# Performance work log

Measured on AMD Instinct MI355X. Metric: run time of the kernel, lower is better.

## Reference

```python
import jax, jax.numpy as jnp
from jax import lax
import numpy as np

DIM, HEADS, R = 256, 8, 2
B, H, W = 4, 64, 64
C = DIM // HEADS
SCALE = C ** -0.5


def setup_inputs() -> dict:
    key = jax.random.key(0)
    ks = jax.random.split(key, 6)
    s = 0.02
    x = jax.random.normal(ks[0], (B, DIM, H, W), dtype=jnp.float32)
    Wq = jax.random.normal(ks[1], (DIM, DIM), dtype=jnp.float32) * s
    Wkv = jax.random.normal(ks[2], (2 * DIM, DIM, R, R), dtype=jnp.float32) * s
    Wqb = jax.random.normal(ks[3], (DIM, DIM), dtype=jnp.float32) * s
    Wkvb = jax.random.normal(ks[4], (2 * DIM, DIM), dtype=jnp.float32) * s
    Wout = jax.random.normal(ks[5], (DIM, DIM), dtype=jnp.float32) * s
    return {"x": x, "Wq": Wq, "Wkv": Wkv, "Wqb": Wqb, "Wkvb": Wkvb, "Wout": Wout}


def _conv1x1(Wm, t):
    # 1x1 conv without bias == channel matmul
    return jnp.einsum('oc,bchw->bohw', Wm, t)


def reference(x, Wq, Wkv, Wqb, Wkvb, Wout):
    b, d, h, w = x.shape
    c = d // HEADS
    # ---- spatial-reduction branch ----
    q = _conv1x1(Wq, x)  # [b, d, h, w]
    kv = lax.conv_general_dilated(x, Wkv, (R, R), 'VALID',
                                  dimension_numbers=('NCHW', 'OIHW', 'NCHW'))
    k, v = jnp.split(kv, 2, axis=1)  # each [b, d, h/R, w/R]

    def to_img(t):
        bb, _, hh, ww = t.shape
        return t.reshape(bb, HEADS, c, hh * ww).transpose(0, 1, 3, 2).reshape(bb * HEADS, hh * ww, c)

    qi, ki, vi = to_img(q), to_img(k), to_img(v)
    attn_img = jax.nn.softmax(jnp.einsum('bid,bjd->bij', qi, ki) * SCALE, axis=-1)
    oi = jnp.einsum('bij,bjd->bid', attn_img, vi)  # [(b h), hw, c]
    out_img = oi.reshape(b, HEADS, h * w, c).transpose(0, 1, 3, 2).reshape(b, d, h, w)

    # ---- batch-wise branch ----
    qb = _conv1x1(Wqb, x)
    kvb = _conv1x1(Wkvb, x)
    kb, vb = jnp.split(kvb, 2, axis=1)

    def to_slice(t):
        # 'b (h c) x y -> (x y h) b c'
        return t.reshape(b, HEADS, c, h * w).transpose(3, 1, 0, 2).reshape(h * w * HEADS, b, c)

    qs, ks_, vs = to_slice(qb), to_slice(kb), to_slice(vb)
    attn_b = jax.nn.softmax(jnp.einsum('ibd,icd->ibc', qs, ks_) * SCALE, axis=-1)
    ob = jnp.einsum('ibc,icd->ibd', attn_b, vs)  # [(hw heads), b, c]
    out_batch = ob.reshape(h * w, HEADS, b, c).transpose(2, 1, 3, 0).reshape(b, d, h, w)

    return _conv1x1(Wout, out_img + out_batch)
```

## Files before the change

### kernel.cpp

```cpp
#include <hip/hip_runtime.h>

#define ATTN_SCALE 0.17677669529663687f

typedef __attribute__((ext_vector_type(8))) short bf16x8;
typedef __attribute__((ext_vector_type(4))) float f32x4;
typedef __attribute__((ext_vector_type(16))) float f32x16;

__device__ inline unsigned short f2bf(float x) {
    unsigned int u = __float_as_uint(x);
    unsigned int r = u + 0x7fffu + ((u >> 16) & 1u);
    return (unsigned short)(r >> 16);
}
__device__ inline unsigned int pk2(float lo, float hi) {
    return (unsigned int)f2bf(lo) | ((unsigned int)f2bf(hi) << 16);
}
__device__ inline float bf2f(unsigned int u) { return __uint_as_float(u << 16); }

#define GLDS16(gp, lp) \
    __builtin_amdgcn_global_load_lds((const __attribute__((address_space(1))) void*)(gp), \
                                     (__attribute__((address_space(3))) void*)(lp), 16, 0, 0)

__device__ inline void stage_tile(const ushort* __restrict__ g, int rstride, int kofs,
                                  ushort* lbase, int w, int lane) {
    const int r0 = w * 32;
    #pragma unroll
    for (int u = 0; u < 4; ++u) {
        const int row  = r0 + u * 8 + (lane >> 3);
        const int slog = (lane & 7) ^ (row & 7);
        GLDS16(g + (size_t)row * rstride + kofs + slog * 8,
               lbase + (size_t)(r0 + u * 8) * 64);
    }
}

__device__ inline bf16x8 frag_ld(const ushort* t, int row, int slog) {
    return *(const bf16x8*)(t + row * 64 + ((slog ^ (row & 7)) * 8));
}

#define MFMA_STEP(WS_, XS_, WM_, WP_)                                                       \
    _Pragma("unroll")                                                                       \
    for (int kh = 0; kh < 2; ++kh) {                                                        \
        bf16x8 av[4], bvv[4];                                                               \
        _Pragma("unroll")                                                                   \
        for (int fm = 0; fm < 4; ++fm) av[fm]  = frag_ld(WS_, WM_ + fm * 16 + i16, kh * 4 + g); \
        _Pragma("unroll")                                                                   \
        for (int fp = 0; fp < 4; ++fp) bvv[fp] = frag_ld(XS_, WP_ + fp * 16 + i16, kh * 4 + g); \
        _Pragma("unroll")                                                                   \
        for (int fm = 0; fm < 4; ++fm)                                                      \
            _Pragma("unroll")                                                               \
            for (int fp = 0; fp < 4; ++fp)                                                  \
                acc[fm][fp] = __builtin_amdgcn_mfma_f32_16x16x32_bf16(av[fm], bvv[fp],      \
                                                                      acc[fm][fp], 0, 0, 0); \
    }

__global__ __launch_bounds__(256) void cvt_x_kernel(
    const float* __restrict__ x, ushort* __restrict__ xbfT)
{
    __shared__ float T[64][65];
    const int t = threadIdx.x;
    const int p0 = blockIdx.x * 64, c0 = blockIdx.y * 64, bb = blockIdx.z;
    const float* xb = x + ((size_t)bb * 256 + c0) * 4096 + p0;
    {
        const int cc = t >> 2, pq = (t & 3) * 16;
        #pragma unroll
        for (int u = 0; u < 4; ++u) {
            const float4 v = *(const float4*)&xb[(size_t)cc * 4096 + pq + u * 4];
            T[cc][pq + u * 4 + 0] = v.x; T[cc][pq + u * 4 + 1] = v.y;
            T[cc][pq + u * 4 + 2] = v.z; T[cc][pq + u * 4 + 3] = v.w;
        }
    }
    __syncthreads();
    {
        const int pp = t >> 2, cq = (t & 3) * 16;
        uint4 w0, w1;
        w0.x = pk2(T[cq + 0][pp],  T[cq + 1][pp]);  w0.y = pk2(T[cq + 2][pp],  T[cq + 3][pp]);
        w0.z = pk2(T[cq + 4][pp],  T[cq + 5][pp]);  w0.w = pk2(T[cq + 6][pp],  T[cq + 7][pp]);
        w1.x = pk2(T[cq + 8][pp],  T[cq + 9][pp]);  w1.y = pk2(T[cq + 10][pp], T[cq + 11][pp]);
        w1.z = pk2(T[cq + 12][pp], T[cq + 13][pp]); w1.w = pk2(T[cq + 14][pp], T[cq + 15][pp]);
        ushort* dst = xbfT + ((size_t)bb * 4096 + p0 + pp) * 256 + c0 + cq;
        *(uint4*)&dst[0] = w0;
        *(uint4*)&dst[8] = w1;
    }
}

__global__ __launch_bounds__(256) void cvt_w_kernel(
    const float* __restrict__ Wq, const float* __restrict__ Wqb,
    const float* __restrict__ Wkvb, const float* __restrict__ Wkv,
    const float* __restrict__ Wout,
    ushort* __restrict__ Wallb, ushort* __restrict__ Wkvbb, ushort* __restrict__ Woutb)
{
    const int id = blockIdx.x * 256 + threadIdx.x;
    const float* src; ushort* dst;
    if (id < 65536) {
        const int m = id >> 6, c4 = (id & 63) * 4;
        src = (m < 256) ? &Wq[(size_t)m * 256 + c4]
            : (m < 512) ? &Wqb[(size_t)(m - 256) * 256 + c4]
                        : &Wkvb[(size_t)(m - 512) * 256 + c4];
        dst = Wallb + (size_t)id * 4;
    } else if (id < 65536 + 131072) {
        const size_t el = (size_t)(id - 65536) * 4;
        src = &Wkv[el]; dst = Wkvbb + el;
    } else if (id < 65536 + 131072 + 16384) {
        const size_t el = (size_t)(id - 65536 - 131072) * 4;
        src = &Wout[el]; dst = Woutb + el;
    } else return;
    const float4 v = *(const float4*)src;
    ushort4 o; o.x = f2bf(v.x); o.y = f2bf(v.y); o.z = f2bf(v.z); o.w = f2bf(v.w);
    *(ushort4*)dst = o;
}

__global__ __launch_bounds__(256) void cvt_xcol_kernel(
    const ushort* __restrict__ xbfT, ushort* __restrict__ xcol)
{
    const int t = threadIdx.x;
    const int bb = blockIdx.y;
    const int pp = blockIdx.x * 4 + (t >> 6);
    const int c0 = (t & 63) * 4;
    const int i = pp >> 5, j = pp & 31;
    const int p00 = i * 128 + 2 * j;
    const ushort* xb = xbfT + (size_t)bb * 4096 * 256;
    const ushort4 r00 = *(const ushort4*)&xb[(size_t)(p00)      * 256 + c0];
    const ushort4 r01 = *(const ushort4*)&xb[(size_t)(p00 + 1)  * 256 + c0];
    const ushort4 r10 = *(const ushort4*)&xb[(size_t)(p00 + 64) * 256 + c0];
    const ushort4 r11 = *(const ushort4*)&xb[(size_t)(p00 + 65) * 256 + c0];
    uint4 w0, w1;
    w0.x = (uint)r00.x | ((uint)r01.x << 16); w0.y = (uint)r10.x | ((uint)r11.x << 16);
    w0.z = (uint)r00.y | ((uint)r01.y << 16); w0.w = (uint)r10.y | ((uint)r11.y << 16);
    w1.x = (uint)r00.z | ((uint)r01.z << 16); w1.y = (uint)r10.z | ((uint)r11.z << 16);
    w1.z = (uint)r00.w | ((uint)r01.w << 16); w1.w = (uint)r10.w | ((uint)r11.w << 16);
    ushort* dst = xcol + ((size_t)bb * 1024 + pp) * 1024 + (size_t)c0 * 4;
    *(uint4*)&dst[0] = w0;
    *(uint4*)&dst[8] = w1;
}

__global__ __launch_bounds__(256) void proj_mfma(
    const ushort* __restrict__ Wallb, const ushort* __restrict__ xbfT,
    ushort* __restrict__ qTb, float* __restrict__ qbT, ushort* __restrict__ kvbT)
{
    __shared__ __align__(16) ushort lds[16384];
    ushort* Ws = lds; ushort* Xs = lds + 8192;
    const int tid = threadIdx.x, lane = tid & 63, w = tid >> 6;
    const int g = lane >> 4, i16 = lane & 15;
    const int p0 = blockIdx.x * 128, m0 = blockIdx.y * 128, bb = blockIdx.z;
    const int wm = (w >> 1) * 64, wp = (w & 1) * 64;
    const ushort* Ag = Wallb + (size_t)m0 * 256;
    const ushort* Bg = xbfT + ((size_t)bb * 4096 + p0) * 256;
    f32x4 acc[4][4] = {};
    for (int ks = 0; ks < 4; ++ks) {
        stage_tile(Ag, 256, ks * 64, Ws, w, lane);
        stage_tile(Bg, 256, ks * 64, Xs, w, lane);
        __syncthreads();
        MFMA_STEP(Ws, Xs, wm, wp);
        __syncthreads();
    }
    #pragma unroll
    for (int fp = 0; fp < 4; ++fp) {
        const int p = p0 + wp + fp * 16 + i16;
        #pragma unroll
        for (int fm = 0; fm < 4; ++fm) {
            const int m = m0 + wm + fm * 16 + 4 * g;
            if (m0 < 256) {
                ushort4 v;
                v.x = f2bf(acc[fm][fp][0] * ATTN_SCALE); v.y = f2bf(acc[fm][fp][1] * ATTN_SCALE);
                v.z = f2bf(acc[fm][fp][2] * ATTN_SCALE); v.w = f2bf(acc[fm][fp][3] * ATTN_SCALE);
                *(ushort4*)&qTb[((size_t)bb * 4096 + p) * 256 + m] = v;
            } else if (m0 < 512) {
                const float4 v = make_float4(acc[fm][fp][0], acc[fm][fp][1],
                                             acc[fm][fp][2], acc[fm][fp][3]);
                *(float4*)&qbT[((size_t)bb * 4096 + p) * 256 + (m - 256)] = v;
            } else {
                ushort4 v;
                v.x = f2bf(acc[fm][fp][0]); v.y = f2bf(acc[fm][fp][1]);
                v.z = f2bf(acc[fm][fp][2]); v.w = f2bf(acc[fm][fp][3]);
                *(ushort4*)&kvbT[((size_t)bb * 4096 + p) * 512 + (m - 512)] = v;
            }
        }
    }
}

__global__ __launch_bounds__(256) void conv_mfma(
    const ushort* __restrict__ Wkvbb, const ushort* __restrict__ xcol,
    ushort* __restrict__ kTb, ushort* __restrict__ vTtb)
{
    __shared__ __align__(16) ushort lds[16384];
    ushort* Ws = lds; ushort* Xs = lds + 8192;
    const int tid = threadIdx.x, lane = tid & 63, w = tid >> 6;
    const int g = lane >> 4, i16 = lane & 15;
    const int pp0 = blockIdx.x * 128, m0 = blockIdx.y * 128, bb = blockIdx.z;
    const int wm = (w >> 1) * 64, wp = (w & 1) * 64;
    const ushort* Ag = Wkvbb + (size_t)m0 * 1024;
    const ushort* Bg = xcol + ((size_t)bb * 1024 + pp0) * 1024;
    f32x4 acc[4][4] = {};
    for (int ks = 0; ks < 16; ++ks) {
        stage_tile(Ag, 1024, ks * 64, Ws, w, lane);
        stage_tile(Bg, 1024, ks * 64, Xs, w, lane);
        __syncthreads();
        MFMA_STEP(Ws, Xs, wm, wp);
        __syncthreads();
    }
    if (m0 < 256) {
        #pragma unroll
        for (int fp = 0; fp < 4; ++fp) {
            const int pp = pp0 + wp + fp * 16 + i16;
            #pragma unroll
            for (int fm = 0; fm < 4; ++fm) {
                const int m = m0 + wm + fm * 16 + 4 * g;
                ushort4 v;
                v.x = f2bf(acc[fm][fp][0]); v.y = f2bf(acc[fm][fp][1]);
                v.z = f2bf(acc[fm][fp][2]); v.w = f2bf(acc[fm][fp][3]);
                *(ushort4*)&kTb[((size_t)bb * 1024 + pp) * 256 + m] = v;
            }
        }
    } else {
        ushort (*T)[128] = (ushort(*)[128])lds;
        #pragma unroll
        for (int fm = 0; fm < 4; ++fm)
            #pragma unroll
            for (int fp = 0; fp < 4; ++fp)
                #pragma unroll
                for (int r = 0; r < 4; ++r)
                    T[wm + fm * 16 + 4 * g + r][wp + fp * 16 + i16] = f2bf(acc[fm][fp][r]);
        __syncthreads();
        #pragma unroll
        for (int u = 0; u < 8; ++u) {
            const int chunk = u * 256 + tid;
            const int row = chunk >> 4, slot = chunk & 15;
            const int mg = m0 - 256 + row;
            const int hh = mg >> 5, cc = mg & 31;
            const uint4 val = *(uint4*)&T[row][slot * 8];
            *(uint4*)&vTtb[((size_t)(bb * 8 + hh) * 32 + cc) * 1024 + pp0 + slot * 8] = val;
        }
    }
}

__global__ __launch_bounds__(256) void out_mfma(
    const float* __restrict__ sumT, const ushort* __restrict__ Woutb,
    float* __restrict__ out)
{
    __shared__ __align__(16) ushort lds[16384];
    ushort* Ss = lds; ushort* Wo = lds + 8192;
    const int tid = threadIdx.x, lane = tid & 63, w = tid >> 6;
    const int g = lane >> 4, i16 = lane & 15;
    const int p0 = blockIdx.x * 128, o0 = blockIdx.y * 128, bb = blockIdx.z;
    const int wpp = (w >> 1) * 64, wo = (w & 1) * 64;
    const float* Sg = sumT + ((size_t)bb * 4096 + p0) * 256;
    const ushort* Bgw = Woutb + (size_t)o0 * 256;
    const int srow = tid >> 1, shalf = tid & 1;
    f32x4 acc[4][4] = {};
    for (int ks = 0; ks < 4; ++ks) {
        {
            const float* src = Sg + (size_t)srow * 256 + ks * 64 + shalf * 32;
            #pragma unroll
            for (int jj = 0; jj < 4; ++jj) {
                const float4 f0 = *(const float4*)&src[jj * 8];
                const float4 f1 = *(const float4*)&src[jj * 8 + 4];
                uint4 pk;
                pk.x = pk2(f0.x, f0.y); pk.y = pk2(f0.z, f0.w);
                pk.z = pk2(f1.x, f1.y); pk.w = pk2(f1.z, f1.w);
                const int slog = shalf * 4 + jj;
                const int sp = slog ^ (srow & 7);
                *(uint4*)&Ss[(size_t)srow * 64 + sp * 8] = pk;
            }
        }
        stage_tile(Bgw, 256, ks * 64, Wo, w, lane);
        __syncthreads();
        MFMA_STEP(Ss, Wo, wpp, wo);
        __syncthreads();
    }
    #pragma unroll
    for (int fo = 0; fo < 4; ++fo) {
        const int o = o0 + wo + fo * 16 + i16;
        #pragma unroll
        for (int fp = 0; fp < 4; ++fp) {
            const int p = p0 + wpp + fp * 16 + 4 * g;
            const float4 v = make_float4(acc[fp][fo][0], acc[fp][fo][1],
                                         acc[fp][fo][2], acc[fp][fo][3]);
            *(float4*)&out[(size_t)bb * 1048576 + (size_t)o * 4096 + p] = v;
        }
    }
}

__global__ __launch_bounds__(256) void attn_img_mfma(
    const ushort* __restrict__ qTb, const ushort* __restrict__ kTb,
    const ushort* __restrict__ vTtb, float* __restrict__ sumT)
{
    __shared__ ushort Ks[128][40];
    __shared__ ushort Vts[32][136];
    const int tid  = threadIdx.x;
    const int lane = tid & 63;
    const int wv   = tid >> 6;
    const int q    = lane & 31;
    const int hi   = lane >> 5;
    const int bh   = blockIdx.x;
    const int b    = bh >> 3, h = bh & 7;
    const int q0   = blockIdx.y * 128 + wv * 32;

    bf16x8 qf[2];
    #pragma unroll
    for (int mm = 0; mm < 2; ++mm)
        qf[mm] = *(const bf16x8*)(qTb + ((size_t)(b * 4096 + q0 + q) * 256 + h * 32 + mm * 16 + hi * 8));

    f32x16 o = {};
    float mrun = -3.0e38f, lrun = 0.f;

    const ushort* kg = kTb + (size_t)b * 1024 * 256 + h * 32;
    const ushort* vg = vTtb + (size_t)bh * 32 * 1024;

    for (int kv0 = 0; kv0 < 1024; kv0 += 128) {
        __syncthreads();
        #pragma unroll
        for (int u = 0; u < 2; ++u) {
            const int chunk = tid + u * 256;
            const int r = chunk >> 2, q4 = chunk & 3;
            *(uint4*)&Ks[r][q4 * 8] = *(const uint4*)(kg + (size_t)(kv0 + r) * 256 + q4 * 8);
            const int c = chunk >> 4, sseg = chunk & 15;
            *(uint4*)&Vts[c][sseg * 8] = *(const uint4*)(vg + (size_t)c * 1024 + kv0 + sseg * 8);
        }
        __syncthreads();

        f32x16 s[4];
        #pragma unroll
        for (int t = 0; t < 4; ++t) {
            const bf16x8 k0 = *(const bf16x8*)&Ks[t * 32 + q][hi * 8];
            const bf16x8 k1 = *(const bf16x8*)&Ks[t * 32 + q][16 + hi * 8];
            f32x16 acc = {};
            acc = __builtin_amdgcn_mfma_f32_32x32x16_bf16(k0, qf[0], acc, 0, 0, 0);
            acc = __builtin_amdgcn_mfma_f32_32x32x16_bf16(k1, qf[1], acc, 0, 0, 0);
            s[t] = acc;
        }
        float pmax = -3.0e38f;
        #pragma unroll
        for (int t = 0; t < 4; ++t)
            #pragma unroll
            for (int r = 0; r < 16; ++r) pmax = fmaxf(pmax, s[t][r]);
        {
            float a_ = pmax, b_ = pmax;
            asm volatile("v_permlane32_swap_b32 %0, %1" : "+v"(a_), "+v"(b_));
            pmax = fmaxf(a_, b_);
        }
        const float mnew  = fmaxf(mrun, pmax);
        const float alpha = __expf(mrun - mnew);
        mrun = mnew;
        float ls = 0.f;
        #pragma unroll
        for (int t = 0; t < 4; ++t)
            #pragma unroll
            for (int r = 0; r < 16; ++r) {
                const float p = __expf(s[t][r] - mnew);
                s[t][r] = p; ls += p;
            }
        {
            float a_ = ls, b_ = ls;
            asm volatile("v_permlane32_swap_b32 %0, %1" : "+v"(a_), "+v"(b_));
            ls = a_ + b_;
        }
        lrun = lrun * alpha + ls;
        #pragma unroll
        for (int r = 0; r < 16; ++r) o[r] *= alpha;

        #pragma unroll
        for (int t = 0; t < 4; ++t) {
            unsigned int W[4][2];
            #pragma unroll
            for (int u = 0; u < 4; ++u) {
                asm("v_cvt_pk_bf16_f32 %0, %1, %2"
                    : "=v"(W[u][0]) : "v"(s[t][4 * u + 0]), "v"(s[t][4 * u + 1]));
                asm("v_cvt_pk_bf16_f32 %0, %1, %2"
                    : "=v"(W[u][1]) : "v"(s[t][4 * u + 2]), "v"(s[t][4 * u + 3]));
            }
            #pragma unroll
            for (int mm = 0; mm < 2; ++mm) {
                unsigned int a0 = W[2 * mm][0], b0 = W[2 * mm + 1][0];
                unsigned int a1 = W[2 * mm][1], b1 = W[2 * mm + 1][1];
                asm volatile("v_permlane32_swap_b32 %0, %1" : "+v"(a0), "+v"(b0));
                asm volatile("v_permlane32_swap_b32 %0, %1" : "+v"(a1), "+v"(b1));
                unsigned int pw[4] = {a0, a1, b0, b1};
                const bf16x8 pf = *(const bf16x8*)pw;
                const bf16x8 vf = *(const bf16x8*)&Vts[q][t * 32 + mm * 16 + hi * 8];
                o = __builtin_amdgcn_mfma_f32_32x32x16_bf16(vf, pf, o, 0, 0, 0);
            }
        }
    }

    const float inv = 1.f / lrun;
    float* dst = sumT + (size_t)(b * 4096 + q0 + q) * 256 + h * 32 + hi * 4;
    #pragma unroll
    for (int u = 0; u < 4; ++u) {
        const float4 v = make_float4(o[4 * u + 0] * inv, o[4 * u + 1] * inv,
                                     o[4 * u + 2] * inv, o[4 * u + 3] * inv);
        *(float4*)&dst[u * 8] = v;
    }
}

__global__ __launch_bounds__(256) void attn_batch_kernel(
    const float* __restrict__ qbT, const ushort* __restrict__ kvbT,
    float* __restrict__ sumT)
{
    const int tid = threadIdx.x;
    const int b1 = tid & 3, h = (tid >> 2) & 7, pl = tid >> 5;
    const int p = blockIdx.x * 8 + pl;

    const float* qrow = qbT + ((size_t)b1 * 4096 + p) * 256 + h * 32;
    float q[32];
    #pragma unroll
    for (int i = 0; i < 8; ++i) {
        const float4 t = ((const float4*)qrow)[i];
        q[4 * i + 0] = t.x * ATTN_SCALE; q[4 * i + 1] = t.y * ATTN_SCALE;
        q[4 * i + 2] = t.z * ATTN_SCALE; q[4 * i + 3] = t.w * ATTN_SCALE;
    }

    float s[4];
    #pragma unroll
    for (int b2 = 0; b2 < 4; ++b2) {
        const uint4* k4 = (const uint4*)(kvbT + ((size_t)b2 * 4096 + p) * 512 + h * 32);
        float d = 0.f;
        #pragma unroll
        for (int i = 0; i < 4; ++i) {
            const uint4 w = k4[i];
            d += q[8 * i + 0] * bf2f(w.x & 0xffffu) + q[8 * i + 1] * bf2f(w.x >> 16);
            d += q[8 * i + 2] * bf2f(w.y & 0xffffu) + q[8 * i + 3] * bf2f(w.y >> 16);
            d += q[8 * i + 4] * bf2f(w.z & 0xffffu) + q[8 * i + 5] * bf2f(w.z >> 16);
            d += q[8 * i + 6] * bf2f(w.w & 0xffffu) + q[8 * i + 7] * bf2f(w.w >> 16);
        }
        s[b2] = d;
    }
    const float mx = fmaxf(fmaxf(s[0], s[1]), fmaxf(s[2], s[3]));
    float w[4];
    float lsum = 0.f;
    #pragma unroll
    for (int b2 = 0; b2 < 4; ++b2) { w[b2] = __expf(s[b2] - mx); lsum += w[b2]; }
    const float inv = 1.f / lsum;
    #pragma unroll
    for (int b2 = 0; b2 < 4; ++b2) w[b2] *= inv;

    float acc[32] = {};
    #pragma unroll
    for (int b2 = 0; b2 < 4; ++b2) {
        const uint4* v4 = (const uint4*)(kvbT + ((size_t)b2 * 4096 + p) * 512 + 256 + h * 32);
        const float wb = w[b2];
        #pragma unroll
        for (int i = 0; i < 4; ++i) {
            const uint4 vv = v4[i];
            acc[8 * i + 0] += wb * bf2f(vv.x & 0xffffu); acc[8 * i + 1] += wb * bf2f(vv.x >> 16);
            acc[8 * i + 2] += wb * bf2f(vv.y & 0xffffu); acc[8 * i + 3] += wb * bf2f(vv.y >> 16);
            acc[8 * i + 4] += wb * bf2f(vv.z & 0xffffu); acc[8 * i + 5] += wb * bf2f(vv.z >> 16);
            acc[8 * i + 6] += wb * bf2f(vv.w & 0xffffu); acc[8 * i + 7] += wb * bf2f(vv.w >> 16);
        }
    }
    float4* o4 = (float4*)(sumT + ((size_t)b1 * 4096 + p) * 256 + h * 32);
    #pragma unroll
    for (int i = 0; i < 8; ++i) {
        float4 c = o4[i];
        c.x += acc[4 * i + 0]; c.y += acc[4 * i + 1];
        c.z += acc[4 * i + 2]; c.w += acc[4 * i + 3];
        o4[i] = c;
    }
}

extern "C" void kernel_launch(void* const* d_in, const int* in_sizes, int n_in,
                              void* d_out, int out_size, void* d_ws, size_t ws_size,
                              hipStream_t stream)
{
    const float* x    = (const float*)d_in[0];
    const float* Wq   = (const float*)d_in[1];
    const float* Wkv  = (const float*)d_in[2];
    const float* Wqb  = (const float*)d_in[3];
    const float* Wkvb = (const float*)d_in[4];
    const float* Wout = (const float*)d_in[5];
    float* out = (float*)d_out;

    ushort* base  = (ushort*)d_ws;
    ushort* xbfT  = base;
    ushort* xcol  = base + 4194304;
    ushort* Wallb = base + 8388608;
    ushort* Wkvbb = base + 8650752;
    float*  sumT  = (float*)base;
    ushort* qTb   = base + 9175040;
    ushort* kvbT  = base + 13369344;
    ushort* kTb   = base + 21757952;
    ushort* vTtb  = base + 22806528;
    ushort* Woutb = base + 23855104;
    float* qbT = out;

    cvt_x_kernel<<<dim3(64, 4, 4), 256, 0, stream>>>(x, xbfT);
    cvt_w_kernel<<<dim3(832), 256, 0, stream>>>(Wq, Wqb, Wkvb, Wkv, Wout, Wallb, Wkvbb, Woutb);
    cvt_xcol_kernel<<<dim3(256, 4), 256, 0, stream>>>(xbfT, xcol);
    proj_mfma<<<dim3(32, 8, 4), 256, 0, stream>>>(Wallb, xbfT, qTb, qbT, kvbT);
    conv_mfma<<<dim3(8, 4, 4), 256, 0, stream>>>(Wkvbb, xcol, kTb, vTtb);
    attn_img_mfma<<<dim3(32, 32), 256, 0, stream>>>(qTb, kTb, vTtb, sumT);
    attn_batch_kernel<<<dim3(512), 256, 0, stream>>>(qbT, kvbT, sumT);
    out_mfma<<<dim3(32, 2, 4), 256, 0, stream>>>(sumT, Woutb, out);
}
```

Before: 131.3 us.

## Prefetch K/V tiles into registers, lazy softmax rescale, exp2 domain, MFMA row-sum

Folds log2(e) into the query scale so the attention kernel can use exp2f directly. The online-softmax rescale now runs only when the running max grows by more than a threshold, checked wave-wide with __any. The row sum is computed by an extra MFMA against a ones vector instead of scalar adds and permlane reductions. The next K/V tile is loaded into registers during compute and written to LDS afterwards. This overlaps global loads with compute at the cost of more registers and an extra MFMA per step, and it relies on the exp2 values staying bounded.

New measurement: 155.1 us. +18.1%, slower.

```diff
diff --git a/kernel.cpp b/kernel.cpp
--- a/kernel.cpp
+++ b/kernel.cpp
@@ -1,6 +1,7 @@
 #include <hip/hip_runtime.h>
 
 #define ATTN_SCALE 0.17677669529663687f
+#define QSCALE (0.17677669529663687f * 1.4426950408889634f)
 
 typedef __attribute__((ext_vector_type(8))) short bf16x8;
 typedef __attribute__((ext_vector_type(4))) float f32x4;
@@ -160,8 +161,8 @@
             const int m = m0 + wm + fm * 16 + 4 * g;
             if (m0 < 256) {
                 ushort4 v;
-                v.x = f2bf(acc[fm][fp][0] * ATTN_SCALE); v.y = f2bf(acc[fm][fp][1] * ATTN_SCALE);
-                v.z = f2bf(acc[fm][fp][2] * ATTN_SCALE); v.w = f2bf(acc[fm][fp][3] * ATTN_SCALE);
+                v.x = f2bf(acc[fm][fp][0] * QSCALE); v.y = f2bf(acc[fm][fp][1] * QSCALE);
+                v.z = f2bf(acc[fm][fp][2] * QSCALE); v.w = f2bf(acc[fm][fp][3] * QSCALE);
                 *(ushort4*)&qTb[((size_t)bb * 4096 + p) * 256 + m] = v;
             } else if (m0 < 512) {
                 const float4 v = make_float4(acc[fm][fp][0], acc[fm][fp][1],
@@ -299,23 +300,41 @@
     for (int mm = 0; mm < 2; ++mm)
         qf[mm] = *(const bf16x8*)(qTb + ((size_t)(b * 4096 + q0 + q) * 256 + h * 32 + mm * 16 + hi * 8));
 
+    unsigned int ow[4] = {0x3f803f80u, 0x3f803f80u, 0x3f803f80u, 0x3f803f80u};
+    const bf16x8 onesf = *(const bf16x8*)ow;
+
     f32x16 o = {};
-    float mrun = -3.0e38f, lrun = 0.f;
+    f32x16 lacc = {};
+    float mrun = -3.0e38f;
 
     const ushort* kg = kTb + (size_t)b * 1024 * 256 + h * 32;
     const ushort* vg = vTtb + (size_t)bh * 32 * 1024;
 
+    const int kr_r = tid >> 2, kq4 = tid & 3;
+    const int vc = tid >> 4, vs = tid & 15;
+    uint4 kr[2], vr[2];
+
+    {
+        kr[0] = *(const uint4*)(kg + (size_t)kr_r * 256 + kq4 * 8);
+        kr[1] = *(const uint4*)(kg + (size_t)(64 + kr_r) * 256 + kq4 * 8);
+        vr[0] = *(const uint4*)(vg + (size_t)vc * 1024 + vs * 8);
+        vr[1] = *(const uint4*)(vg + (size_t)(16 + vc) * 1024 + vs * 8);
+        *(uint4*)&Ks[kr_r][kq4 * 8]      = kr[0];
+        *(uint4*)&Ks[64 + kr_r][kq4 * 8] = kr[1];
+        *(uint4*)&Vts[vc][vs * 8]        = vr[0];
+        *(uint4*)&Vts[16 + vc][vs * 8]   = vr[1];
+    }
+    __syncthreads();
+
     for (int kv0 = 0; kv0 < 1024; kv0 += 128) {
-        __syncthreads();
-        #pragma unroll
-        for (int u = 0; u < 2; ++u) {
-            const int chunk = tid + u * 256;
-            const int r = chunk >> 2, q4 = chunk & 3;
-            *(uint4*)&Ks[r][q4 * 8] = *(const uint4*)(kg + (size_t)(kv0 + r) * 256 + q4 * 8);
-            const int c = chunk >> 4, sseg = chunk & 15;
-            *(uint4*)&Vts[c][sseg * 8] = *(const uint4*)(vg + (size_t)c * 1024 + kv0 + sseg * 8);
-        }
-        __syncthreads();
+        const bool more = kv0 < 896;
+        if (more) {
+            const int nx = kv0 + 128;
+            kr[0] = *(const uint4*)(kg + (size_t)(nx + kr_r) * 256 + kq4 * 8);
+            kr[1] = *(const uint4*)(kg + (size_t)(nx + 64 + kr_r) * 256 + kq4 * 8);
+            vr[0] = *(const uint4*)(vg + (size_t)vc * 1024 + nx + vs * 8);
+            vr[1] = *(const uint4*)(vg + (size_t)(16 + vc) * 1024 + nx + vs * 8);
+        }
 
         f32x16 s[4];
         #pragma unroll
@@ -327,38 +346,34 @@
             acc = __builtin_amdgcn_mfma_f32_32x32x16_bf16(k1, qf[1], acc, 0, 0, 0);
             s[t] = acc;
         }
-        float pmax = -3.0e38f;
-        #pragma unroll
-        for (int t = 0; t < 4; ++t)
-            #pragma unroll
-            for (int r = 0; r < 16; ++r) pmax = fmaxf(pmax, s[t][r]);
+        float v8[8];
+        #pragma unroll
+        for (int t = 0; t < 4; ++t) {
+            v8[2 * t]     = fmaxf(fmaxf(fmaxf(s[t][0], s[t][1]), fmaxf(s[t][2], s[t][3])),
+                                  fmaxf(fmaxf(s[t][4], s[t][5]), fmaxf(s[t][6], s[t][7])));
+            v8[2 * t + 1] = fmaxf(fmaxf(fmaxf(s[t][8], s[t][9]), fmaxf(s[t][10], s[t][11])),
+                                  fmaxf(fmaxf(s[t][12], s[t][13]), fmaxf(s[t][14], s[t][15])));
+        }
+        float pmax = fmaxf(fmaxf(fmaxf(v8[0], v8[1]), fmaxf(v8[2], v8[3])),
+                           fmaxf(fmaxf(v8[4], v8[5]), fmaxf(v8[6], v8[7])));
         {
             float a_ = pmax, b_ = pmax;
             asm volatile("v_permlane32_swap_b32 %0, %1" : "+v"(a_), "+v"(b_));
             pmax = fmaxf(a_, b_);
         }
-        const float mnew  = fmaxf(mrun, pmax);
-        const float alpha = __expf(mrun - mnew);
-        mrun = mnew;
-        float ls = 0.f;
-        #pragma unroll
-        for (int t = 0; t < 4; ++t)
-            #pragma unroll
-            for (int r = 0; r < 16; ++r) {
-                const float p = __expf(s[t][r] - mnew);
-                s[t][r] = p; ls += p;
-            }
-        {
-            float a_ = ls, b_ = ls;
-            asm volatile("v_permlane32_swap_b32 %0, %1" : "+v"(a_), "+v"(b_));
-            ls = a_ + b_;
-        }
-        lrun = lrun * alpha + ls;
-        #pragma unroll
-        for (int r = 0; r < 16; ++r) o[r] *= alpha;
+        if (__any(pmax > mrun + 12.0f)) {
+            const float mnew = fmaxf(mrun, pmax);
+            const float al = exp2f(mrun - mnew);
+            mrun = mnew;
+            #pragma unroll
+            for (int r = 0; r < 16; ++r) o[r] *= al;
+            lacc[0] *= al;
+        }
 
         #pragma unroll
         for (int t = 0; t < 4; ++t) {
+            #pragma unroll
+            for (int r = 0; r < 16; ++r) s[t][r] = exp2f(s[t][r] - mrun);
             unsigned int W[4][2];
             #pragma unroll
             for (int u = 0; u < 4; ++u) {
@@ -377,11 +392,21 @@
                 const bf16x8 pf = *(const bf16x8*)pw;
                 const bf16x8 vf = *(const bf16x8*)&Vts[q][t * 32 + mm * 16 + hi * 8];
                 o = __builtin_amdgcn_mfma_f32_32x32x16_bf16(vf, pf, o, 0, 0, 0);
+                lacc = __builtin_amdgcn_mfma_f32_32x32x16_bf16(onesf, pf, lacc, 0, 0, 0);
             }
         }
-    }
-
-    const float inv = 1.f / lrun;
+
+        if (more) {
+            __syncthreads();
+            *(uint4*)&Ks[kr_r][kq4 * 8]      = kr[0];
+            *(uint4*)&Ks[64 + kr_r][kq4 * 8] = kr[1];
+            *(uint4*)&Vts[vc][vs * 8]        = vr[0];
+            *(uint4*)&Vts[16 + vc][vs * 8]   = vr[1];
+            __syncthreads();
+        }
+    }
+
+    const float inv = 1.f / lacc[0];
     float* dst = sumT + (size_t)(b * 4096 + q0 + q) * 256 + h * 32 + hi * 4;
     #pragma unroll
     for (int u = 0; u < 4; ++u) {
```

## Use exp2 with folded log2e, lazy rescaling, and MFMA row-sum in image attention

Applied to the files above, without the earlier changes.

Folds log2(e) into the Q scaling so the softmax can use exp2f directly. The online max is now updated per 32-key subtile, and the accumulator is rescaled only when some lane's max grows by more than 12 (in log2 units). The row sum is computed with an extra MFMA against a ones vector rather than a scalar sum plus a cross-lane swap. This cuts VALU exp, reduction and rescale work, but adds one MFMA per P·V step and allows probabilities up to 2^12 before rescaling, which carries some bf16 and overflow risk.

Result: slower. 143.1 us (+9.0%).

```diff
diff --git a/kernel.cpp b/kernel.cpp
--- a/kernel.cpp
+++ b/kernel.cpp
@@ -1,6 +1,7 @@
 #include <hip/hip_runtime.h>
 
 #define ATTN_SCALE 0.17677669529663687f
+#define QSCALE (0.17677669529663687f * 1.4426950408889634f)
 
 typedef __attribute__((ext_vector_type(8))) short bf16x8;
 typedef __attribute__((ext_vector_type(4))) float f32x4;
@@ -160,8 +161,8 @@
             const int m = m0 + wm + fm * 16 + 4 * g;
             if (m0 < 256) {
                 ushort4 v;
-                v.x = f2bf(acc[fm][fp][0] * ATTN_SCALE); v.y = f2bf(acc[fm][fp][1] * ATTN_SCALE);
-                v.z = f2bf(acc[fm][fp][2] * ATTN_SCALE); v.w = f2bf(acc[fm][fp][3] * ATTN_SCALE);
+                v.x = f2bf(acc[fm][fp][0] * QSCALE); v.y = f2bf(acc[fm][fp][1] * QSCALE);
+                v.z = f2bf(acc[fm][fp][2] * QSCALE); v.w = f2bf(acc[fm][fp][3] * QSCALE);
                 *(ushort4*)&qTb[((size_t)bb * 4096 + p) * 256 + m] = v;
             } else if (m0 < 512) {
                 const float4 v = make_float4(acc[fm][fp][0], acc[fm][fp][1],
@@ -299,8 +300,12 @@
     for (int mm = 0; mm < 2; ++mm)
         qf[mm] = *(const bf16x8*)(qTb + ((size_t)(b * 4096 + q0 + q) * 256 + h * 32 + mm * 16 + hi * 8));
 
+    unsigned int ow[4] = {0x3f803f80u, 0x3f803f80u, 0x3f803f80u, 0x3f803f80u};
+    const bf16x8 onesf = *(const bf16x8*)ow;
+
     f32x16 o = {};
-    float mrun = -3.0e38f, lrun = 0.f;
+    f32x16 lacc = {};
+    float mrun = -3.0e38f;
 
     const ushort* kg = kTb + (size_t)b * 1024 * 256 + h * 32;
     const ushort* vg = vTtb + (size_t)bh * 32 * 1024;
@@ -317,55 +322,42 @@
         }
         __syncthreads();
 
-        f32x16 s[4];
         #pragma unroll
         for (int t = 0; t < 4; ++t) {
             const bf16x8 k0 = *(const bf16x8*)&Ks[t * 32 + q][hi * 8];
             const bf16x8 k1 = *(const bf16x8*)&Ks[t * 32 + q][16 + hi * 8];
-            f32x16 acc = {};
-            acc = __builtin_amdgcn_mfma_f32_32x32x16_bf16(k0, qf[0], acc, 0, 0, 0);
-            acc = __builtin_amdgcn_mfma_f32_32x32x16_bf16(k1, qf[1], acc, 0, 0, 0);
-            s[t] = acc;
-        }
-        float pmax = -3.0e38f;
-        #pragma unroll
-        for (int t = 0; t < 4; ++t)
-            #pragma unroll
-            for (int r = 0; r < 16; ++r) pmax = fmaxf(pmax, s[t][r]);
-        {
-            float a_ = pmax, b_ = pmax;
-            asm volatile("v_permlane32_swap_b32 %0, %1" : "+v"(a_), "+v"(b_));
-            pmax = fmaxf(a_, b_);
-        }
-        const float mnew  = fmaxf(mrun, pmax);
-        const float alpha = __expf(mrun - mnew);
-        mrun = mnew;
-        float ls = 0.f;
-        #pragma unroll
-        for (int t = 0; t < 4; ++t)
-            #pragma unroll
-            for (int r = 0; r < 16; ++r) {
-                const float p = __expf(s[t][r] - mnew);
-                s[t][r] = p; ls += p;
-            }
-        {
-            float a_ = ls, b_ = ls;
-            asm volatile("v_permlane32_swap_b32 %0, %1" : "+v"(a_), "+v"(b_));
-            ls = a_ + b_;
-        }
-        lrun = lrun * alpha + ls;
-        #pragma unroll
-        for (int r = 0; r < 16; ++r) o[r] *= alpha;
-
-        #pragma unroll
-        for (int t = 0; t < 4; ++t) {
+            f32x16 s = {};
+            s = __builtin_amdgcn_mfma_f32_32x32x16_bf16(k0, qf[0], s, 0, 0, 0);
+            s = __builtin_amdgcn_mfma_f32_32x32x16_bf16(k1, qf[1], s, 0, 0, 0);
+
+            float m0_ = fmaxf(fmaxf(s[0], s[1]), fmaxf(s[2], s[3]));
+            float m1_ = fmaxf(fmaxf(s[4], s[5]), fmaxf(s[6], s[7]));
+            float m2_ = fmaxf(fmaxf(s[8], s[9]), fmaxf(s[10], s[11]));
+            float m3_ = fmaxf(fmaxf(s[12], s[13]), fmaxf(s[14], s[15]));
+            float pmax = fmaxf(fmaxf(m0_, m1_), fmaxf(m2_, m3_));
+            {
+                float a_ = pmax, b_ = pmax;
+                asm volatile("v_permlane32_swap_b32 %0, %1" : "+v"(a_), "+v"(b_));
+                pmax = fmaxf(a_, b_);
+            }
+            if (__any(pmax > mrun + 12.0f)) {
+                const float mnew = fmaxf(mrun, pmax);
+                const float al = exp2f(mrun - mnew);
+                mrun = mnew;
+                #pragma unroll
+                for (int r = 0; r < 16; ++r) o[r] *= al;
+                lacc[0] *= al;
+            }
+            #pragma unroll
+            for (int r = 0; r < 16; ++r) s[r] = exp2f(s[r] - mrun);
+
             unsigned int W[4][2];
             #pragma unroll
             for (int u = 0; u < 4; ++u) {
                 asm("v_cvt_pk_bf16_f32 %0, %1, %2"
-                    : "=v"(W[u][0]) : "v"(s[t][4 * u + 0]), "v"(s[t][4 * u + 1]));
+                    : "=v"(W[u][0]) : "v"(s[4 * u + 0]), "v"(s[4 * u + 1]));
                 asm("v_cvt_pk_bf16_f32 %0, %1, %2"
-                    : "=v"(W[u][1]) : "v"(s[t][4 * u + 2]), "v"(s[t][4 * u + 3]));
+                    : "=v"(W[u][1]) : "v"(s[4 * u + 2]), "v"(s[4 * u + 3]));
             }
             #pragma unroll
             for (int mm = 0; mm < 2; ++mm) {
@@ -377,11 +369,12 @@
                 const bf16x8 pf = *(const bf16x8*)pw;
                 const bf16x8 vf = *(const bf16x8*)&Vts[q][t * 32 + mm * 16 + hi * 8];
                 o = __builtin_amdgcn_mfma_f32_32x32x16_bf16(vf, pf, o, 0, 0, 0);
-            }
-        }
-    }
-
-    const float inv = 1.f / lrun;
+                lacc = __builtin_amdgcn_mfma_f32_32x32x16_bf16(onesf, pf, lacc, 0, 0, 0);
+            }
+        }
+    }
+
+    const float inv = 1.f / lacc[0];
     float* dst = sumT + (size_t)(b * 4096 + q0 + q) * 256 + h * 32 + hi * 4;
     #pragma unroll
     for (int u = 0; u < 4; ++u) {
```
